# Optimization experiments

Measured on AMD Instinct MI355X. Metric: run time of the kernel, lower is better.

Reference implementation:

```python
import jax, jax.numpy as jnp
import numpy as np

D_MODEL = 1024
NUM_HEADS = 16
D_K = D_MODEL // NUM_HEADS


def setup_inputs() -> dict:
    key = jax.random.key(0)
    ks = jax.random.split(key, 11)
    B, S = 4, 2048
    s = 1.0 / np.sqrt(D_MODEL)
    return {
        "Q": jax.random.normal(ks[0], (B, S, D_MODEL), jnp.float32),
        "K": jax.random.normal(ks[1], (B, S, D_MODEL), jnp.float32),
        "V": jax.random.normal(ks[2], (B, S, D_MODEL), jnp.float32),
        "Wq": jax.random.normal(ks[3], (D_MODEL, D_MODEL), jnp.float32) * s,
        "bq": jax.random.normal(ks[4], (D_MODEL,), jnp.float32) * 0.01,
        "Wk": jax.random.normal(ks[5], (D_MODEL, D_MODEL), jnp.float32) * s,
        "bk": jax.random.normal(ks[6], (D_MODEL,), jnp.float32) * 0.01,
        "Wv": jax.random.normal(ks[7], (D_MODEL, D_MODEL), jnp.float32) * s,
        "bv": jax.random.normal(ks[8], (D_MODEL,), jnp.float32) * 0.01,
        "Wo": jax.random.normal(ks[9], (D_MODEL, D_MODEL), jnp.float32) * s,
        "bo": jax.random.normal(ks[10], (D_MODEL,), jnp.float32) * 0.01,
    }


def _split_heads(x):
    B, S, _ = x.shape
    return x.reshape(B, S, NUM_HEADS, D_K).transpose(0, 2, 1, 3)  # [B,H,S,Dk]


def reference(Q, K, V, Wq, bq, Wk, bk, Wv, bv, Wo, bo):
    # Linear layers (torch nn.Linear: x @ W.T + b)
    q = _split_heads(Q @ Wq.T + bq)
    k = _split_heads(K @ Wk.T + bk)
    v = _split_heads(V @ Wv.T + bv)
    scale = 1.0 / jnp.sqrt(jnp.asarray(D_K, jnp.float32))
    scores = jnp.einsum('bhqd,bhkd->bhqk', q, k) * scale  # [B,H,S,S]
    attn = jax.nn.softmax(scores, axis=-1)
    ctx = jnp.einsum('bhqk,bhkd->bhqd', attn, v)  # [B,H,S,Dk]
    B, H, S, Dk = ctx.shape
    ctx = ctx.transpose(0, 2, 1, 3).reshape(B, S, H * Dk)
    return ctx @ Wo.T + bo
```

## Files before the change

### kernel.cpp

```cpp
#include <hip/hip_runtime.h>
#include <hip/hip_bf16.h>

#define B_SZ 4
#define S_SZ 2048
#define D_SZ 1024
#define H_SZ 16
#define DK_SZ 64
#define M_ROWS (B_SZ * S_SZ)

typedef __bf16 bf16x8 __attribute__((ext_vector_type(8)));
typedef __bf16 bf16x4 __attribute__((ext_vector_type(4)));
typedef float  f32x4  __attribute__((ext_vector_type(4)));

typedef __attribute__((address_space(3))) unsigned int lds_u32;
typedef const __attribute__((address_space(1))) unsigned int glob_u32;

__device__ __forceinline__ bf16x8 load8(const float* p) {
    f32x4 a = *(const f32x4*)p;
    f32x4 b = *(const f32x4*)(p + 4);
    bf16x8 r;
    r[0] = (__bf16)a[0]; r[1] = (__bf16)a[1]; r[2] = (__bf16)a[2]; r[3] = (__bf16)a[3];
    r[4] = (__bf16)b[0]; r[5] = (__bf16)b[1]; r[6] = (__bf16)b[2]; r[7] = (__bf16)b[3];
    return r;
}
__device__ __forceinline__ bf16x8 load8(const __bf16* p) {
    return *(const bf16x8*)p;
}

__global__ __launch_bounds__(256)
void conv_bf16(const float* __restrict__ in, __bf16* __restrict__ out, int n8) {
    int i = blockIdx.x * 256 + threadIdx.x;
    const int stride = gridDim.x * 256;
    for (; i < n8; i += stride)
        *(bf16x8*)&out[(size_t)i * 8] = load8(in + (size_t)i * 8);
}

template <typename TC>
__global__ __launch_bounds__(256, 2)
void gemm_nt_bias_g(const __bf16* __restrict__ A, const __bf16* __restrict__ W,
                    const float* __restrict__ bias, TC* __restrict__ C,
                    int M, int N, int K) {
    __shared__ __align__(16) __bf16 sA[2][128 * 64];
    __shared__ __align__(16) __bf16 sB[2][128 * 64];
    const int tid = threadIdx.x;
    const int w = tid >> 6, lane = tid & 63;

    int mt, nt;
    if (gridDim.x == 64 && gridDim.y == 8) {
        const int lin = blockIdx.x + blockIdx.y * 64;
        const int xcd = lin & 7, idx = lin >> 3;
        mt = xcd * 8 + (idx >> 3);
        nt = idx & 7;
    } else { mt = blockIdx.x; nt = blockIdx.y; }
    const int m0 = mt * 128, n0 = nt * 128;

    const int wr = w >> 1, wc = w & 1;
    const int lr = lane & 15, lq = lane >> 4;

    const int st_roff = lane >> 3;
    const int st_cg   = (lane & 7) ^ st_roff;

    f32x4 acc[4][4] = {};

    auto STAGE = [&](int kt, int bsel) {
#pragma unroll
        for (int i = 0; i < 4; ++i) {
            const int seg = i * 4 + w;
            const int row = seg * 8 + st_roff;
            __builtin_amdgcn_global_load_lds(
                (glob_u32*)(A + (size_t)(m0 + row) * K + kt + st_cg * 8),
                (lds_u32*)(&sA[bsel][seg * 512]), 16, 0, 0);
            __builtin_amdgcn_global_load_lds(
                (glob_u32*)(W + (size_t)(n0 + row) * K + kt + st_cg * 8),
                (lds_u32*)(&sB[bsel][seg * 512]), 16, 0, 0);
        }
    };
    auto COMPUTE = [&](int bsel) {
#pragma unroll
        for (int s = 0; s < 2; ++s) {
            bf16x8 av[4], bv[4];
#pragma unroll
            for (int i = 0; i < 4; ++i)
                av[i] = *(const bf16x8*)&sA[bsel][(wr * 64 + i * 16 + lr) * 64
                                                  + (((s * 4 + lq) ^ (lr & 7)) << 3)];
#pragma unroll
            for (int j = 0; j < 4; ++j)
                bv[j] = *(const bf16x8*)&sB[bsel][(wc * 64 + j * 16 + lr) * 64
                                                  + (((s * 4 + lq) ^ (lr & 7)) << 3)];
#pragma unroll
            for (int i = 0; i < 4; ++i)
#pragma unroll
                for (int j = 0; j < 4; ++j)
                    acc[i][j] = __builtin_amdgcn_mfma_f32_16x16x32_bf16(
                        av[i], bv[j], acc[i][j], 0, 0, 0);
        }
    };

    STAGE(0, 0);
    __syncthreads();
    int buf = 0;
    for (int kt = 64; kt < K; kt += 64) {
        STAGE(kt, buf ^ 1);
        COMPUTE(buf);
        __syncthreads();
        buf ^= 1;
    }
    COMPUTE(buf);

#pragma unroll
    for (int j = 0; j < 4; ++j) {
        const int col = n0 + wc * 64 + j * 16 + lr;
        const float bias_f = bias[col];
#pragma unroll
        for (int i = 0; i < 4; ++i) {
            const int rbase = m0 + wr * 64 + i * 16 + lq * 4;
#pragma unroll
            for (int r = 0; r < 4; ++r)
                C[(size_t)(rbase + r) * N + col] = (TC)(acc[i][j][r] + bias_f);
        }
    }
}

#define SAST 72
template <typename TA, typename TW, typename TC>
__global__ __launch_bounds__(256, 2)
void gemm_nt_bias(const TA* __restrict__ A, const TW* __restrict__ W,
                  const float* __restrict__ bias, TC* __restrict__ C,
                  int M, int N, int K) {
    __shared__ __align__(16) __bf16 sA[128 * SAST];
    __shared__ __align__(16) __bf16 sB[128 * SAST];
    const int tid = threadIdx.x;
    const int w = tid >> 6, lane = tid & 63;
    const int m0 = blockIdx.x * 128, n0 = blockIdx.y * 128;
    const int wr = w >> 1, wc = w & 1;
    const int lr = lane & 15, lq = lane >> 4;

    f32x4 acc[4][4] = {};

    for (int kt = 0; kt < K; kt += 64) {
        for (int it = 0; it < 4; ++it) {
            const int c = it * 256 + tid;
            const int row = c >> 3, col8 = c & 7;
            *(bf16x8*)&sA[row * SAST + col8 * 8] =
                load8(A + (size_t)(m0 + row) * K + kt + col8 * 8);
            *(bf16x8*)&sB[row * SAST + col8 * 8] =
                load8(W + (size_t)(n0 + row) * K + kt + col8 * 8);
        }
        __syncthreads();
        for (int s = 0; s < 2; ++s) {
            bf16x8 av[4], bv[4];
            for (int i = 0; i < 4; ++i)
                av[i] = *(const bf16x8*)&sA[(wr * 64 + i * 16 + lr) * SAST + s * 32 + lq * 8];
            for (int j = 0; j < 4; ++j)
                bv[j] = *(const bf16x8*)&sB[(wc * 64 + j * 16 + lr) * SAST + s * 32 + lq * 8];
            for (int i = 0; i < 4; ++i)
                for (int j = 0; j < 4; ++j)
                    acc[i][j] = __builtin_amdgcn_mfma_f32_16x16x32_bf16(
                        av[i], bv[j], acc[i][j], 0, 0, 0);
        }
        __syncthreads();
    }
    for (int j = 0; j < 4; ++j) {
        const int col = n0 + wc * 64 + j * 16 + lr;
        const float bias_f = bias[col];
        for (int i = 0; i < 4; ++i) {
            const int rbase = m0 + wr * 64 + i * 16 + lq * 4;
            for (int r = 0; r < 4; ++r)
                C[(size_t)(rbase + r) * N + col] = (TC)(acc[i][j][r] + bias_f);
        }
    }
}

#define KVB 64
#define PST 72
__global__ __launch_bounds__(256, 2)
void attn_kernel(const __bf16* qm, const __bf16* __restrict__ km,
                 const __bf16* __restrict__ vm, __bf16* ctx) {
    __shared__ __align__(16) __bf16 sK[KVB * 64];
    __shared__ __align__(16) __bf16 sVt[64 * KVB];
    __shared__ __align__(16) __bf16 sP[8][16 * PST];

    const int tid = threadIdx.x, w = tid >> 6, lane = tid & 63;
    const int lr = lane & 15, lq = lane >> 4;
    const int bh = blockIdx.y, b = bh >> 4, h = bh & 15;
    const int q0 = blockIdx.x * 128;
    const size_t rowbase = (size_t)b * S_SZ;
    const int hoff = h * DK_SZ;

    bf16x8 qf[2][2];
#pragma unroll
    for (int qs = 0; qs < 2; ++qs) {
        const __bf16* qp = qm + (rowbase + q0 + w * 32 + qs * 16 + lr) * D_SZ + hoff;
        qf[qs][0] = *(const bf16x8*)(qp + lq * 8);
        qf[qs][1] = *(const bf16x8*)(qp + 32 + lq * 8);
    }

    float mrow[2] = {-1e30f, -1e30f};
    float lrow[2] = {0.f, 0.f};
    f32x4 o[2][4] = {};

    const int gl_koff = (lane >> 3);
    const int gl_c8 = lane & 7;
    const int v_key7 = tid >> 3, v_d8 = tid & 7;

    const __bf16* kbase = km + rowbase * D_SZ + hoff;
    const __bf16* vbase = vm + rowbase * D_SZ + hoff;

    for (int k0 = 0; k0 < S_SZ; k0 += KVB) {
#pragma unroll
        for (int i = 0; i < 2; ++i) {
            const int key = w * 16 + i * 8 + gl_koff;
            const __bf16* gp = kbase + (size_t)(k0 + key) * D_SZ
                               + ((gl_c8 ^ gl_koff) << 3);
            __builtin_amdgcn_global_load_lds(
                (glob_u32*)gp, (lds_u32*)(&sK[(w * 2 + i) * 512]), 16, 0, 0);
        }
#pragma unroll
        for (int p = 0; p < 2; ++p) {
            const int key = p * 32 + v_key7;
            bf16x8 vv = *(const bf16x8*)(vbase + (size_t)(k0 + key) * D_SZ + (v_d8 << 3));
            const int colbase = (((key >> 3) ^ v_d8) << 3) + (key & 7);
#pragma unroll
            for (int e = 0; e < 8; ++e)
                sVt[(v_d8 * 8 + e) * 64 + colbase] = vv[e];
        }
        __syncthreads();

        f32x4 sc[2][4] = {};
#pragma unroll
        for (int s = 0; s < 2; ++s) {
            bf16x8 kf[4];
#pragma unroll
            for (int nt = 0; nt < 4; ++nt)
                kf[nt] = *(const bf16x8*)&sK[(nt * 16 + lr) * 64
                                             + (((s * 4 + lq) ^ (lr & 7)) << 3)];
#pragma unroll
            for (int nt = 0; nt < 4; ++nt) {
                sc[0][nt] = __builtin_amdgcn_mfma_f32_16x16x32_bf16(
                    kf[nt], qf[0][s], sc[0][nt], 0, 0, 0);
                sc[1][nt] = __builtin_amdgcn_mfma_f32_16x16x32_bf16(
                    kf[nt], qf[1][s], sc[1][nt], 0, 0, 0);
            }
        }

#pragma unroll
        for (int qs = 0; qs < 2; ++qs) {
            float sv[4][4];
            float mt = -1e30f;
#pragma unroll
            for (int nt = 0; nt < 4; ++nt)
#pragma unroll
                for (int r = 0; r < 4; ++r) {
                    sv[nt][r] = sc[qs][nt][r] * 0.125f;
                    mt = fmaxf(mt, sv[nt][r]);
                }
            mt = fmaxf(mt, __shfl_xor(mt, 16));
            mt = fmaxf(mt, __shfl_xor(mt, 32));
            if (!__all(mt - mrow[qs] <= 8.f)) {
                const float mn = fmaxf(mrow[qs], mt);
                const float al = __expf(mrow[qs] - mn);
                mrow[qs] = mn;
                lrow[qs] *= al;
                float a4[4];
#pragma unroll
                for (int r = 0; r < 4; ++r)
                    a4[r] = __shfl(al, ((lane >> 4) << 2) + r, 64);
#pragma unroll
                for (int nt = 0; nt < 4; ++nt)
#pragma unroll
                    for (int r = 0; r < 4; ++r)
                        o[qs][nt][r] *= a4[r];
            }
            float ls = 0.f;
#pragma unroll
            for (int nt = 0; nt < 4; ++nt) {
                bf16x4 pk;
#pragma unroll
                for (int r = 0; r < 4; ++r) {
                    const float pv = __expf(sv[nt][r] - mrow[qs]);
                    ls += pv;
                    pk[r] = (__bf16)pv;
                }
                *(bf16x4*)&sP[w * 2 + qs][lr * PST + nt * 16 + lq * 4] = pk;
            }
            ls += __shfl_xor(ls, 16);
            ls += __shfl_xor(ls, 32);
            lrow[qs] += ls;
        }

        bf16x8 pf[2][2];
#pragma unroll
        for (int qs = 0; qs < 2; ++qs)
#pragma unroll
            for (int s = 0; s < 2; ++s)
                pf[qs][s] = *(const bf16x8*)&sP[w * 2 + qs][lr * PST + s * 32 + lq * 8];
#pragma unroll
        for (int s = 0; s < 2; ++s)
#pragma unroll
            for (int nt = 0; nt < 4; ++nt) {
                bf16x8 vf = *(const bf16x8*)&sVt[
                    (nt * 16 + lr) * 64
                    + (((s * 4 + lq) ^ (nt * 2 + (lr >> 3))) << 3)];
                o[0][nt] = __builtin_amdgcn_mfma_f32_16x16x32_bf16(
                    pf[0][s], vf, o[0][nt], 0, 0, 0);
                o[1][nt] = __builtin_amdgcn_mfma_f32_16x16x32_bf16(
                    pf[1][s], vf, o[1][nt], 0, 0, 0);
            }
        __syncthreads();
    }

#pragma unroll
    for (int qs = 0; qs < 2; ++qs) {
        const float linv = 1.f / lrow[qs];
        float l4[4];
#pragma unroll
        for (int r = 0; r < 4; ++r)
            l4[r] = __shfl(linv, ((lane >> 4) << 2) + r, 64);
#pragma unroll
        for (int nt = 0; nt < 4; ++nt) {
            const int col = hoff + nt * 16 + lr;
#pragma unroll
            for (int r = 0; r < 4; ++r) {
                const size_t row = rowbase + q0 + w * 32 + qs * 16 + lq * 4 + r;
                ctx[row * D_SZ + col] = (__bf16)(o[qs][nt][r] * l4[r]);
            }
        }
    }
}

extern "C" void kernel_launch(void* const* d_in, const int* in_sizes, int n_in,
                              void* d_out, int out_size, void* d_ws, size_t ws_size,
                              hipStream_t stream) {
    const float* Q  = (const float*)d_in[0];
    const float* K  = (const float*)d_in[1];
    const float* V  = (const float*)d_in[2];
    const float* Wq = (const float*)d_in[3];
    const float* bq = (const float*)d_in[4];
    const float* Wk = (const float*)d_in[5];
    const float* bk = (const float*)d_in[6];
    const float* Wv = (const float*)d_in[7];
    const float* bv = (const float*)d_in[8];
    const float* Wo = (const float*)d_in[9];
    const float* bo = (const float*)d_in[10];
    float* out = (float*)d_out;

    const size_t plane = (size_t)M_ROWS * D_SZ;
    const size_t wsz   = (size_t)D_SZ * D_SZ;
    const dim3 gg(M_ROWS / 128, D_SZ / 128), bb(256);
    const dim3 ag(S_SZ / 128, B_SZ * H_SZ);

    const size_t need_fast = (3 * plane + 4 * wsz) * sizeof(__bf16);
    if (ws_size >= need_fast) {
        __bf16* s0  = (__bf16*)d_ws;
        __bf16* qw  = s0 + plane;
        __bf16* kw  = s0 + 2 * plane;
        __bf16* wgt = s0 + 3 * plane;
        __bf16* vw  = (__bf16*)d_out;
        const int p8 = (int)(plane / 8), w8 = (int)(wsz / 8);

        conv_bf16<<<512, bb, 0, stream>>>(Wq, wgt, w8);
        conv_bf16<<<512, bb, 0, stream>>>(Wk, wgt + wsz, w8);
        conv_bf16<<<512, bb, 0, stream>>>(Wv, wgt + 2 * wsz, w8);
        conv_bf16<<<512, bb, 0, stream>>>(Wo, wgt + 3 * wsz, w8);

        conv_bf16<<<2048, bb, 0, stream>>>(Q, s0, p8);
        gemm_nt_bias_g<__bf16><<<gg, bb, 0, stream>>>(
            s0, wgt, bq, qw, M_ROWS, D_SZ, D_SZ);
        conv_bf16<<<2048, bb, 0, stream>>>(K, s0, p8);
        gemm_nt_bias_g<__bf16><<<gg, bb, 0, stream>>>(
            s0, wgt + wsz, bk, kw, M_ROWS, D_SZ, D_SZ);
        conv_bf16<<<2048, bb, 0, stream>>>(V, s0, p8);
        gemm_nt_bias_g<__bf16><<<gg, bb, 0, stream>>>(
            s0, wgt + 2 * wsz, bv, vw, M_ROWS, D_SZ, D_SZ);

        attn_kernel<<<ag, bb, 0, stream>>>(qw, kw, vw, qw);

        gemm_nt_bias_g<float><<<gg, bb, 0, stream>>>(
            qw, wgt + 3 * wsz, bo, out, M_ROWS, D_SZ, D_SZ);
        return;
    }

    if (ws_size < 2 * plane * sizeof(__bf16)) return;
    __bf16* qw = (__bf16*)d_ws;
    __bf16* kw = qw + plane;
    __bf16* vw = (__bf16*)d_out;
    __bf16* cw = qw;

    gemm_nt_bias<float, float, __bf16><<<gg, bb, 0, stream>>>(Q, Wq, bq, qw, M_ROWS, D_SZ, D_SZ);
    gemm_nt_bias<float, float, __bf16><<<gg, bb, 0, stream>>>(K, Wk, bk, kw, M_ROWS, D_SZ, D_SZ);
    gemm_nt_bias<float, float, __bf16><<<gg, bb, 0, stream>>>(V, Wv, bv, vw, M_ROWS, D_SZ, D_SZ);

    attn_kernel<<<ag, bb, 0, stream>>>(qw, kw, vw, cw);

    gemm_nt_bias<__bf16, float, float><<<gg, bb, 0, stream>>>(cw, Wo, bo, out,
                                                              M_ROWS, D_SZ, D_SZ);
}
```

Baseline: 393.7 us.

## Double-buffer K/V tiles in attention and remap blocks for XCD locality

Adds two LDS buffers for K and transposed V, so the next tile's K loads (async global-to-LDS) and V register prefetch are issued before computing on the current tile. This cuts one barrier per iteration and hides global load latency behind MFMA work. It also remaps the block index so blocks sharing a batch-head land on the same XCD, which should improve L2 reuse of K/V. LDS use doubles, which may reduce occupancy, and more registers are live because of the held V prefetch.

Result: no change. 392.7 us (-0.3%).

```diff
diff --git a/kernel.cpp b/kernel.cpp
--- a/kernel.cpp
+++ b/kernel.cpp
@@ -176,14 +176,22 @@
 __global__ __launch_bounds__(256, 2)
 void attn_kernel(const __bf16* qm, const __bf16* __restrict__ km,
                  const __bf16* __restrict__ vm, __bf16* ctx) {
-    __shared__ __align__(16) __bf16 sK[KVB * 64];
-    __shared__ __align__(16) __bf16 sVt[64 * KVB];
+    __shared__ __align__(16) __bf16 sK[2][KVB * 64];
+    __shared__ __align__(16) __bf16 sVt[2][64 * KVB];
     __shared__ __align__(16) __bf16 sP[8][16 * PST];
 
     const int tid = threadIdx.x, w = tid >> 6, lane = tid & 63;
     const int lr = lane & 15, lq = lane >> 4;
-    const int bh = blockIdx.y, b = bh >> 4, h = bh & 15;
-    const int q0 = blockIdx.x * 128;
+
+    int qblk, bh;
+    if (gridDim.x == 16 && gridDim.y == 64) {
+        const int lin = blockIdx.x + blockIdx.y * 16;
+        const int xcd = lin & 7, idx = lin >> 3;
+        bh = xcd * 8 + (idx >> 4);
+        qblk = idx & 15;
+    } else { qblk = blockIdx.x; bh = blockIdx.y; }
+    const int b = bh >> 4, h = bh & 15;
+    const int q0 = qblk * 128;
     const size_t rowbase = (size_t)b * S_SZ;
     const int hoff = h * DK_SZ;
 
@@ -202,29 +210,44 @@
     const int gl_koff = (lane >> 3);
     const int gl_c8 = lane & 7;
     const int v_key7 = tid >> 3, v_d8 = tid & 7;
+    const int cb0 = (((v_key7 >> 3) ^ v_d8) << 3) + (v_key7 & 7);
+    const int cb1 = ((((32 + v_key7) >> 3) ^ v_d8) << 3) + (v_key7 & 7);
 
     const __bf16* kbase = km + rowbase * D_SZ + hoff;
     const __bf16* vbase = vm + rowbase * D_SZ + hoff;
 
-    for (int k0 = 0; k0 < S_SZ; k0 += KVB) {
+    auto stageK = [&](int k0t, int bsel) {
 #pragma unroll
         for (int i = 0; i < 2; ++i) {
             const int key = w * 16 + i * 8 + gl_koff;
-            const __bf16* gp = kbase + (size_t)(k0 + key) * D_SZ
+            const __bf16* gp = kbase + (size_t)(k0t + key) * D_SZ
                                + ((gl_c8 ^ gl_koff) << 3);
             __builtin_amdgcn_global_load_lds(
-                (glob_u32*)gp, (lds_u32*)(&sK[(w * 2 + i) * 512]), 16, 0, 0);
-        }
-#pragma unroll
-        for (int p = 0; p < 2; ++p) {
-            const int key = p * 32 + v_key7;
-            bf16x8 vv = *(const bf16x8*)(vbase + (size_t)(k0 + key) * D_SZ + (v_d8 << 3));
-            const int colbase = (((key >> 3) ^ v_d8) << 3) + (key & 7);
-#pragma unroll
-            for (int e = 0; e < 8; ++e)
-                sVt[(v_d8 * 8 + e) * 64 + colbase] = vv[e];
-        }
-        __syncthreads();
+                (glob_u32*)gp, (lds_u32*)(&sK[bsel][(w * 2 + i) * 512]), 16, 0, 0);
+        }
+    };
+
+    stageK(0, 0);
+    {
+        bf16x8 a0 = *(const bf16x8*)(vbase + (size_t)(v_key7) * D_SZ + (v_d8 << 3));
+        bf16x8 a1 = *(const bf16x8*)(vbase + (size_t)(32 + v_key7) * D_SZ + (v_d8 << 3));
+#pragma unroll
+        for (int e = 0; e < 8; ++e) {
+            sVt[0][(v_d8 * 8 + e) * 64 + cb0] = a0[e];
+            sVt[0][(v_d8 * 8 + e) * 64 + cb1] = a1[e];
+        }
+    }
+    __syncthreads();
+
+    int buf = 0;
+    for (int k0 = 0; k0 < S_SZ; k0 += KVB) {
+        const bool more = (k0 + KVB) < S_SZ;
+        bf16x8 nv0, nv1;
+        if (more) {
+            stageK(k0 + KVB, buf ^ 1);
+            nv0 = *(const bf16x8*)(vbase + (size_t)(k0 + KVB + v_key7) * D_SZ + (v_d8 << 3));
+            nv1 = *(const bf16x8*)(vbase + (size_t)(k0 + KVB + 32 + v_key7) * D_SZ + (v_d8 << 3));
+        }
 
         f32x4 sc[2][4] = {};
 #pragma unroll
@@ -232,8 +255,8 @@
             bf16x8 kf[4];
 #pragma unroll
             for (int nt = 0; nt < 4; ++nt)
-                kf[nt] = *(const bf16x8*)&sK[(nt * 16 + lr) * 64
-                                             + (((s * 4 + lq) ^ (lr & 7)) << 3)];
+                kf[nt] = *(const bf16x8*)&sK[buf][(nt * 16 + lr) * 64
+                                                  + (((s * 4 + lq) ^ (lr & 7)) << 3)];
 #pragma unroll
             for (int nt = 0; nt < 4; ++nt) {
                 sc[0][nt] = __builtin_amdgcn_mfma_f32_16x16x32_bf16(
@@ -298,7 +321,7 @@
         for (int s = 0; s < 2; ++s)
 #pragma unroll
             for (int nt = 0; nt < 4; ++nt) {
-                bf16x8 vf = *(const bf16x8*)&sVt[
+                bf16x8 vf = *(const bf16x8*)&sVt[buf][
                     (nt * 16 + lr) * 64
                     + (((s * 4 + lq) ^ (nt * 2 + (lr >> 3))) << 3)];
                 o[0][nt] = __builtin_amdgcn_mfma_f32_16x16x32_bf16(
@@ -306,7 +329,16 @@
                 o[1][nt] = __builtin_amdgcn_mfma_f32_16x16x32_bf16(
                     pf[1][s], vf, o[1][nt], 0, 0, 0);
             }
-        __syncthreads();
+
+        if (more) {
+#pragma unroll
+            for (int e = 0; e < 8; ++e) {
+                sVt[buf ^ 1][(v_d8 * 8 + e) * 64 + cb0] = nv0[e];
+                sVt[buf ^ 1][(v_d8 * 8 + e) * 64 + cb1] = nv1[e];
+            }
+            __syncthreads();
+        }
+        buf ^= 1;
     }
 
 #pragma unroll
```
